# Kernel optimization log

Hardware: AMD Instinct MI355X
Metric: run time of the kernel (lower is better)

Reference implementation:

```python
import jax, jax.numpy as jnp
import numpy as np

GRID_H = 64
GRID_W = 64


def make_grid(h, w):
    # torch.meshgrid([arange(h), arange(w)], indexing='xy') -> shape (w, h);
    # grid[i, j] = (j + 0.5, i + 0.5). With h == w == 64 this is square.
    gx, gy = jnp.meshgrid(jnp.arange(h, dtype=jnp.float32),
                          jnp.arange(w, dtype=jnp.float32), indexing='xy')
    return jnp.stack([gx, gy], axis=-1) + 0.5  # (w, h, 2)


def setup_inputs() -> dict:
    key = jax.random.key(0)
    k1, k2 = jax.random.split(key)
    x = jax.random.normal(k1, (4, 128, 64, 64), dtype=jnp.float32)
    y = jax.random.normal(k2, (4, 128, 64, 64), dtype=jnp.float32)
    return {"x": x, "y": y}


def reference(x, y):
    b, c, hx, wx = x.shape
    _, _, hy, wy = y.shape
    scale = c ** (-0.5)
    grids = make_grid(GRID_H, GRID_W)[:hy, :wy].reshape(-1, 2)  # (hy*wy, 2)

    x_ = x.reshape(b, c, hx * wx)
    y_ = y.reshape(b, c, hy * wy)
    # (b, q, k) attention over all key pixels
    attn = jax.nn.softmax(jnp.einsum('bcq,bck->bqk', x_, y_) * scale, axis=-1)
    uv = jnp.einsum('bqk,kt->bqt', attn, grids)  # (b, hx*wx, 2)
    uv = uv.reshape(b, hx, wx, 2)
    # normalize to [-1, 1]
    norm = jnp.asarray([wy, hy], dtype=uv.dtype)
    uv = uv / norm * 2.0 - 1.0
    return uv
```

## Files before the change

### kernel.cpp

```cpp
#include <hip/hip_runtime.h>
#include <math.h>

typedef __attribute__((ext_vector_type(8))) _Float16 f16x8;
typedef __attribute__((ext_vector_type(4))) float f32x4;

#define NPIX 4096
#define C_DIM 128
#define SCALE2 0.12752064638518208f

#if __has_builtin(__builtin_amdgcn_exp2f)
#define EXP2(x) __builtin_amdgcn_exp2f(x)
#else
#define EXP2(x) exp2f(x)
#endif

#define WS_NEED ((size_t)4 << 20)

__global__ __launch_bounds__(256) void conv_y(const float* __restrict__ y,
                                              char* __restrict__ ws)
{
    __shared__ float T[32][132];
    const int wg  = blockIdx.x;
    const int xcd = wg & 7;
    const int b   = xcd >> 1;
    const int sl  = ((xcd & 1) << 6) | (wg >> 3);
    const int k0  = sl * 32;
    const int t   = threadIdx.x;

    {
        const int c = t >> 1, half = t & 1;
        const float* srow = y + ((size_t)b * C_DIM + c) * NPIX + k0 + half * 16;
        float4 rv[4];
        #pragma unroll
        for (int u = 0; u < 4; ++u) rv[u] = *(const float4*)(srow + u * 4);
        #pragma unroll
        for (int u = 0; u < 4; ++u) {
            T[half * 16 + u * 4 + 0][c] = rv[u].x;
            T[half * 16 + u * 4 + 1][c] = rv[u].y;
            T[half * 16 + u * 4 + 2][c] = rv[u].z;
            T[half * 16 + u * 4 + 3][c] = rv[u].w;
        }
    }
    __syncthreads();

    char* panel = ws + (size_t)b * (NPIX * 256);
    const int k = t >> 3, g2 = t & 7;
    f16x8 v0, v1;
    #pragma unroll
    for (int m = 0; m < 8; ++m) {
        v0[m] = (_Float16)T[k][g2 * 16 + m];
        v1[m] = (_Float16)T[k][g2 * 16 + 8 + m];
    }
    const int key = k0 + k, s = key & 7;
    char* drow = panel + (size_t)key * 256;
    *(f16x8*)(drow + (((2 * g2)     ^ s) << 4)) = v0;
    *(f16x8*)(drow + (((2 * g2 + 1) ^ s) << 4)) = v1;
}

__global__ __launch_bounds__(1024) void uv_main(const char* __restrict__ ws,
                                                const float* __restrict__ x,
                                                float* __restrict__ out)
{
    __shared__ __align__(16) char Ys[2][65536];
    __shared__ float red[16][64][3];

    const int t = threadIdx.x, w = t >> 6, l = t & 63;
    const int n16 = l & 15, quad = l >> 4;
    const int wg  = blockIdx.x;
    const int xcd = wg & 7;
    const int b   = xcd >> 1;
    const int qt  = ((xcd & 1) << 5) | (wg >> 3);
    const int q0  = qt * 64;

    const char* panel = ws + (size_t)b * (NPIX * 256);

    int soff[4];
    #pragma unroll
    for (int i = 0; i < 4; ++i) soff[i] = (w * 16 + i * 4) * 256 + l * 16;

    #pragma unroll
    for (int i = 0; i < 4; ++i)
        __builtin_amdgcn_global_load_lds(
            (const __attribute__((address_space(1))) void*)(panel + soff[i]),
            (__attribute__((address_space(3))) void*)(&Ys[0][soff[i]]), 16, 0, 0);

    f16x8 bx[4][4];
    {
        const float* xq = x + (size_t)b * C_DIM * NPIX + q0 + n16;
        #pragma unroll
        for (int cc = 0; cc < 4; ++cc)
            #pragma unroll
            for (int qg = 0; qg < 4; ++qg) {
                f16x8 hh;
                #pragma unroll
                for (int j = 0; j < 8; ++j)
                    hh[j] = (_Float16)(xq[(size_t)(cc * 32 + quad * 8 + j) * NPIX + qg * 16] * SCALE2);
                bx[cc][qg] = hh;
            }
    }

    const int arow = w * 16 + n16;
    int aoff[4];
    #pragma unroll
    for (int cc = 0; cc < 4; ++cc)
        aoff[cc] = arow * 256 + (((cc * 4 + quad) ^ (n16 & 7)) << 4);

    float gxv[4];
    #pragma unroll
    for (int r = 0; r < 4; ++r) gxv[r] = (float)((w & 3) * 16 + quad * 4 + r) + 0.5f;
    const float gyw = (float)(w >> 2) + 0.5f;
    float den[4] = {0.f, 0.f, 0.f, 0.f}, nu[4] = {0.f, 0.f, 0.f, 0.f}, nv[4] = {0.f, 0.f, 0.f, 0.f};

    #pragma unroll 1
    for (int kt = 0; kt < 16; ++kt) {
        char* cur = Ys[kt & 1];

        if (kt < 15) {
            const char* gt = panel + (size_t)(kt + 1) * 65536;
            char* nb = Ys[(kt + 1) & 1];
            #pragma unroll
            for (int i = 0; i < 4; ++i)
                __builtin_amdgcn_global_load_lds(
                    (const __attribute__((address_space(1))) void*)(gt + soff[i]),
                    (__attribute__((address_space(3))) void*)(&nb[soff[i]]), 16, 0, 0);
            __builtin_amdgcn_s_waitcnt(0x0F74);
        } else {
            __builtin_amdgcn_s_waitcnt(0x0F70);
        }

        const float gy = 4.0f * (float)kt + gyw;

        f16x8 A[4];
        #pragma unroll
        for (int cc = 0; cc < 4; ++cc)
            A[cc] = *(const f16x8*)(cur + aoff[cc]);

        {
            f32x4 acc0 = (f32x4){0.f, 0.f, 0.f, 0.f};
            f32x4 acc1 = (f32x4){0.f, 0.f, 0.f, 0.f};
            #pragma unroll
            for (int cc = 0; cc < 4; ++cc) {
                acc0 = __builtin_amdgcn_mfma_f32_16x16x32_f16(A[cc], bx[cc][0], acc0, 0, 0, 0);
                acc1 = __builtin_amdgcn_mfma_f32_16x16x32_f16(A[cc], bx[cc][1], acc1, 0, 0, 0);
            }
            float ps0 = 0.f, pc0 = 0.f, ps1 = 0.f, pc1 = 0.f;
            #pragma unroll
            for (int r = 0; r < 4; ++r) {
                const float p0 = EXP2(acc0[r]);
                const float p1 = EXP2(acc1[r]);
                ps0 += p0; pc0 += p0 * gxv[r];
                ps1 += p1; pc1 += p1 * gxv[r];
            }
            den[0] += ps0; nu[0] += pc0; nv[0] += gy * ps0;
            den[1] += ps1; nu[1] += pc1; nv[1] += gy * ps1;
        }
        {
            f32x4 acc0 = (f32x4){0.f, 0.f, 0.f, 0.f};
            f32x4 acc1 = (f32x4){0.f, 0.f, 0.f, 0.f};
            #pragma unroll
            for (int cc = 0; cc < 4; ++cc) {
                acc0 = __builtin_amdgcn_mfma_f32_16x16x32_f16(A[cc], bx[cc][2], acc0, 0, 0, 0);
                acc1 = __builtin_amdgcn_mfma_f32_16x16x32_f16(A[cc], bx[cc][3], acc1, 0, 0, 0);
            }
            float ps0 = 0.f, pc0 = 0.f, ps1 = 0.f, pc1 = 0.f;
            #pragma unroll
            for (int r = 0; r < 4; ++r) {
                const float p0 = EXP2(acc0[r]);
                const float p1 = EXP2(acc1[r]);
                ps0 += p0; pc0 += p0 * gxv[r];
                ps1 += p1; pc1 += p1 * gxv[r];
            }
            den[2] += ps0; nu[2] += pc0; nv[2] += gy * ps0;
            den[3] += ps1; nu[3] += pc1; nv[3] += gy * ps1;
        }
    }

    #pragma unroll
    for (int qg = 0; qg < 4; ++qg) {
        #pragma unroll
        for (int mk = 16; mk <= 32; mk <<= 1) {
            den[qg] += __shfl_xor(den[qg], mk);
            nu[qg]  += __shfl_xor(nu[qg],  mk);
            nv[qg]  += __shfl_xor(nv[qg],  mk);
        }
    }
    if (quad == 0) {
        #pragma unroll
        for (int qg = 0; qg < 4; ++qg) {
            red[w][qg * 16 + n16][0] = den[qg];
            red[w][qg * 16 + n16][1] = nu[qg];
            red[w][qg * 16 + n16][2] = nv[qg];
        }
    }
    __syncthreads();
    if (t < 64) {
        float d = 0.f, u = 0.f, v = 0.f;
        #pragma unroll
        for (int ww = 0; ww < 16; ++ww) {
            d += red[ww][t][0];
            u += red[ww][t][1];
            v += red[ww][t][2];
        }
        const float inv = 1.0f / d;
        *(float2*)(out + ((size_t)b * NPIX + q0 + t) * 2) =
            make_float2(u * inv * 0.03125f - 1.0f, v * inv * 0.03125f - 1.0f);
    }
}

__global__ __launch_bounds__(256, 2) void uv_attn_kernel(
    const float* __restrict__ x, const float* __restrict__ y, float* __restrict__ out)
{
    __shared__ float Xs[C_DIM][32];
    __shared__ float Ysf[64][128];
    const float SCALE = 0.08838834764831845f;
    const int tid = threadIdx.x;
    const int wgid = blockIdx.x;
    const int xcd = wgid & 7;
    const int b = xcd & 3;
    const int q0 = (((xcd >> 2) << 6) | (wgid >> 3)) * 32;
    const float* xb = x + (size_t)b * C_DIM * NPIX + q0;
    {
        const int cr = tid >> 3;
        const int cc = (tid & 7) << 2;
        #pragma unroll
        for (int i = 0; i < 4; ++i) {
            float4 v = *(const float4*)(xb + (size_t)(cr + (i << 5)) * NPIX + cc);
            v.x *= SCALE; v.y *= SCALE; v.z *= SCALE; v.w *= SCALE;
            *(float4*)(&Xs[cr + (i << 5)][cc]) = v;
        }
    }
    const int rg = tid >> 4;
    const int lane16 = tid & 15;
    const int r0 = rg << 1;
    const int col0 = lane16 << 3;
    float gxv[8];
    #pragma unroll
    for (int j2 = 0; j2 < 8; ++j2) gxv[j2] = (float)((col0 & 63) + j2) + 0.5f;
    const float gyb = (float)(lane16 >> 3) + 0.5f;
    float m_run[2] = {-INFINITY, -INFINITY};
    float den[2] = {0.f, 0.f}, nu[2] = {0.f, 0.f}, nv[2] = {0.f, 0.f};
    const int yr = tid >> 5;
    const int yc = (tid & 31) << 2;
    const float* ybase = y + (size_t)b * C_DIM * NPIX;
    for (int kt = 0; kt < 32; ++kt) {
        float S[2][8];
        #pragma unroll
        for (int r = 0; r < 2; ++r)
            #pragma unroll
            for (int j2 = 0; j2 < 8; ++j2) S[r][j2] = 0.f;
        #pragma unroll
        for (int cb = 0; cb < 2; ++cb) {
            __syncthreads();
            const float* yt = ybase + (size_t)(cb << 6) * NPIX + kt * 128;
            #pragma unroll
            for (int i = 0; i < 8; ++i)
                *(float4*)(&Ysf[yr + (i << 3)][yc]) =
                    *(const float4*)(yt + (size_t)(yr + (i << 3)) * NPIX + yc);
            __syncthreads();
            const int cbase = cb << 6;
            #pragma unroll 16
            for (int c = 0; c < 64; ++c) {
                const float2 xa = *(const float2*)(&Xs[cbase + c][r0]);
                const float4 ya = *(const float4*)(&Ysf[c][col0]);
                const float4 yb4 = *(const float4*)(&Ysf[c][col0 + 4]);
                S[0][0] += xa.x * ya.x;  S[0][1] += xa.x * ya.y;
                S[0][2] += xa.x * ya.z;  S[0][3] += xa.x * ya.w;
                S[0][4] += xa.x * yb4.x; S[0][5] += xa.x * yb4.y;
                S[0][6] += xa.x * yb4.z; S[0][7] += xa.x * yb4.w;
                S[1][0] += xa.y * ya.x;  S[1][1] += xa.y * ya.y;
                S[1][2] += xa.y * ya.z;  S[1][3] += xa.y * ya.w;
                S[1][4] += xa.y * yb4.x; S[1][5] += xa.y * yb4.y;
                S[1][6] += xa.y * yb4.z; S[1][7] += xa.y * yb4.w;
            }
        }
        const float gy = gyb + 2.0f * (float)kt;
        #pragma unroll
        for (int r = 0; r < 2; ++r) {
            float tmax = S[r][0];
            #pragma unroll
            for (int j2 = 1; j2 < 8; ++j2) tmax = fmaxf(tmax, S[r][j2]);
            #pragma unroll
            for (int mk = 8; mk >= 1; mk >>= 1) tmax = fmaxf(tmax, __shfl_xor(tmax, mk, 16));
            const float mnew = fmaxf(m_run[r], tmax);
            const float alpha = __expf(m_run[r] - mnew);
            m_run[r] = mnew;
            float psum = 0.f, pu = 0.f;
            #pragma unroll
            for (int j2 = 0; j2 < 8; ++j2) {
                const float p = __expf(S[r][j2] - mnew);
                psum += p; pu += p * gxv[j2];
            }
            den[r] = den[r] * alpha + psum;
            nu[r] = nu[r] * alpha + pu;
            nv[r] = nv[r] * alpha + gy * psum;
        }
    }
    #pragma unroll
    for (int r = 0; r < 2; ++r)
        #pragma unroll
        for (int mk = 8; mk >= 1; mk >>= 1) {
            den[r] += __shfl_xor(den[r], mk, 16);
            nu[r] += __shfl_xor(nu[r], mk, 16);
            nv[r] += __shfl_xor(nv[r], mk, 16);
        }
    if (lane16 == 0) {
        #pragma unroll
        for (int r = 0; r < 2; ++r) {
            const float inv = 1.0f / den[r];
            const int q = q0 + r0 + r;
            *(float2*)(out + ((size_t)b * NPIX + q) * 2) =
                make_float2(nu[r] * inv * 0.03125f - 1.0f, nv[r] * inv * 0.03125f - 1.0f);
        }
    }
}

extern "C" void kernel_launch(void* const* d_in, const int* in_sizes, int n_in,
                              void* d_out, int out_size, void* d_ws, size_t ws_size,
                              hipStream_t stream) {
    const float* x = (const float*)d_in[0];
    const float* y = (const float*)d_in[1];
    float* out = (float*)d_out;
    if (ws_size >= WS_NEED) {
        hipLaunchKernelGGL(conv_y, dim3(512), dim3(256), 0, stream, y, (char*)d_ws);
        hipLaunchKernelGGL(uv_main, dim3(256), dim3(1024), 0, stream,
                           (const char*)d_ws, x, out);
    } else {
        hipLaunchKernelGGL(uv_attn_kernel, dim3(512), dim3(256), 0, stream, x, y, out);
    }
}
```

Measured before the change: 93.34 us.

## Fuse y conversion into main kernel with a grid-wide atomic barrier

Drops the separate conv_y launch. Each of the 256 workgroups in the main kernel now converts its own 64-key slice of y to swizzled fp16 in the workspace. A grid-wide barrier, built on a monotonically increasing atomic counter, then makes the workgroups wait for one another before they load the panel, and the x loads overlap the wait. This removes a kernel launch and the gap between kernels. In exchange it relies on all 256 workgroups being resident at once, which deadlocks otherwise, and it adds spin-wait cost on the critical path.

```diff
diff --git a/kernel.cpp b/kernel.cpp
--- a/kernel.cpp
+++ b/kernel.cpp
@@ -16,50 +16,12 @@
 
 #define WS_NEED ((size_t)4 << 20)
 
-__global__ __launch_bounds__(256) void conv_y(const float* __restrict__ y,
-                                              char* __restrict__ ws)
-{
-    __shared__ float T[32][132];
-    const int wg  = blockIdx.x;
-    const int xcd = wg & 7;
-    const int b   = xcd >> 1;
-    const int sl  = ((xcd & 1) << 6) | (wg >> 3);
-    const int k0  = sl * 32;
-    const int t   = threadIdx.x;
-
-    {
-        const int c = t >> 1, half = t & 1;
-        const float* srow = y + ((size_t)b * C_DIM + c) * NPIX + k0 + half * 16;
-        float4 rv[4];
-        #pragma unroll
-        for (int u = 0; u < 4; ++u) rv[u] = *(const float4*)(srow + u * 4);
-        #pragma unroll
-        for (int u = 0; u < 4; ++u) {
-            T[half * 16 + u * 4 + 0][c] = rv[u].x;
-            T[half * 16 + u * 4 + 1][c] = rv[u].y;
-            T[half * 16 + u * 4 + 2][c] = rv[u].z;
-            T[half * 16 + u * 4 + 3][c] = rv[u].w;
-        }
-    }
-    __syncthreads();
-
-    char* panel = ws + (size_t)b * (NPIX * 256);
-    const int k = t >> 3, g2 = t & 7;
-    f16x8 v0, v1;
-    #pragma unroll
-    for (int m = 0; m < 8; ++m) {
-        v0[m] = (_Float16)T[k][g2 * 16 + m];
-        v1[m] = (_Float16)T[k][g2 * 16 + 8 + m];
-    }
-    const int key = k0 + k, s = key & 7;
-    char* drow = panel + (size_t)key * 256;
-    *(f16x8*)(drow + (((2 * g2)     ^ s) << 4)) = v0;
-    *(f16x8*)(drow + (((2 * g2 + 1) ^ s) << 4)) = v1;
-}
-
-__global__ __launch_bounds__(1024) void uv_main(const char* __restrict__ ws,
-                                                const float* __restrict__ x,
-                                                float* __restrict__ out)
+__device__ unsigned bar_ctr = 0;
+
+__global__ __launch_bounds__(1024) void uv_all(char* __restrict__ ws,
+                                               const float* __restrict__ x,
+                                               const float* __restrict__ y,
+                                               float* __restrict__ out)
 {
     __shared__ __align__(16) char Ys[2][65536];
     __shared__ float red[16][64][3];
@@ -72,17 +34,40 @@
     const int qt  = ((xcd & 1) << 5) | (wg >> 3);
     const int q0  = qt * 64;
 
-    const char* panel = ws + (size_t)b * (NPIX * 256);
-
-    int soff[4];
-    #pragma unroll
-    for (int i = 0; i < 4; ++i) soff[i] = (w * 16 + i * 4) * 256 + l * 16;
-
-    #pragma unroll
-    for (int i = 0; i < 4; ++i)
-        __builtin_amdgcn_global_load_lds(
-            (const __attribute__((address_space(1))) void*)(panel + soff[i]),
-            (__attribute__((address_space(3))) void*)(&Ys[0][soff[i]]), 16, 0, 0);
+    char* panel = ws + (size_t)b * (NPIX * 256);
+
+    {
+        const int k0 = qt * 64;
+        float* T = (float*)&Ys[0][0];
+
+        {
+            const int c = t >> 3, grp = t & 7;
+            const float* srow = y + ((size_t)b * C_DIM + c) * NPIX + k0 + grp * 8;
+            const float4 r0 = *(const float4*)(srow);
+            const float4 r1 = *(const float4*)(srow + 4);
+            float* Tb = T + (size_t)(grp * 8) * 130 + c;
+            Tb[0 * 130] = r0.x; Tb[1 * 130] = r0.y; Tb[2 * 130] = r0.z; Tb[3 * 130] = r0.w;
+            Tb[4 * 130] = r1.x; Tb[5 * 130] = r1.y; Tb[6 * 130] = r1.z; Tb[7 * 130] = r1.w;
+        }
+        __syncthreads();
+        {
+            const int kk = t >> 4, gi = t & 15;
+            const float* Tr = T + (size_t)kk * 130 + gi * 8;
+            f16x8 v;
+            #pragma unroll
+            for (int m = 0; m < 8; ++m) v[m] = (_Float16)Tr[m];
+            const int key = k0 + kk, s = key & 7;
+            *(f16x8*)(panel + (size_t)key * 256 + ((gi ^ s) << 4)) = v;
+        }
+        __syncthreads();
+    }
+
+    unsigned target = 0;
+    if (t == 0) {
+        __threadfence();
+        const unsigned ticket = atomicAdd(&bar_ctr, 1u);
+        target = (ticket >> 8) * 256u + 256u;
+    }
 
     f16x8 bx[4][4];
     {
@@ -98,6 +83,23 @@
                 bx[cc][qg] = hh;
             }
     }
+
+    if (t == 0) {
+        while (__hip_atomic_load(&bar_ctr, __ATOMIC_RELAXED, __HIP_MEMORY_SCOPE_AGENT) < target)
+            __builtin_amdgcn_s_sleep(8);
+        __threadfence();
+    }
+    __syncthreads();
+
+    int soff[4];
+    #pragma unroll
+    for (int i = 0; i < 4; ++i) soff[i] = (w * 16 + i * 4) * 256 + l * 16;
+
+    #pragma unroll
+    for (int i = 0; i < 4; ++i)
+        __builtin_amdgcn_global_load_lds(
+            (const __attribute__((address_space(1))) void*)(panel + soff[i]),
+            (__attribute__((address_space(3))) void*)(&Ys[0][soff[i]]), 16, 0, 0);
 
     const int arow = w * 16 + n16;
     int aoff[4];
@@ -321,9 +323,8 @@
     const float* y = (const float*)d_in[1];
     float* out = (float*)d_out;
     if (ws_size >= WS_NEED) {
-        hipLaunchKernelGGL(conv_y, dim3(512), dim3(256), 0, stream, y, (char*)d_ws);
-        hipLaunchKernelGGL(uv_main, dim3(256), dim3(1024), 0, stream,
-                           (const char*)d_ws, x, out);
+        hipLaunchKernelGGL(uv_all, dim3(256), dim3(1024), 0, stream,
+                           (char*)d_ws, x, y, out);
     } else {
         hipLaunchKernelGGL(uv_attn_kernel, dim3(512), dim3(256), 0, stream, x, y, out);
     }
```

Result: slower. 109.6 us (+17.4%).
